# Optimization experiments

Hardware: AMD Instinct MI355X
Metric: run time of the kernel (lower is better)

## Reference

```python
import jax, jax.numpy as jnp
import numpy as np

IN_F = 4096
OUT_F = 11008

def setup_inputs() -> dict:
    key = jax.random.key(0)
    k1, k2, k3, k4 = jax.random.split(key, 4)
    x = jax.random.normal(k1, (4, 128, IN_F), dtype=jnp.float32)
    # int8-style quantized weights stored as int32 in [-127, 127]
    quantized_weight = jax.random.randint(k2, (OUT_F, IN_F), -127, 128, dtype=jnp.int32)
    # per-output-row scale, kept away from zero
    scale = jax.random.uniform(k3, (OUT_F, 1), dtype=jnp.float32, minval=0.5, maxval=1.5)
    bias = jax.random.normal(k4, (OUT_F,), dtype=jnp.float32)
    return {"x": x, "quantized_weight": quantized_weight, "scale": scale, "bias": bias}

def reference(x, quantized_weight, scale, bias):
    # int8 dequantization: weight = q.float() / scale  -> [OUT_F, IN_F] fp32
    weight = quantized_weight.astype(jnp.float32) / scale
    # F.linear(x, weight, bias) == x @ weight.T + bias
    out = jnp.einsum('bsi,oi->bso', x, weight) + bias
    return out
```

## Files before the change

### kernel.cpp

```cpp
#include <hip/hip_runtime.h>
#include <hip/hip_bf16.h>
#include <stdint.h>

#define IN_F  4096
#define OUT_F 11008
#define MTOT  512

#define BM 128
#define BN 64
#define BK 64
#define NKT (IN_F / BK)
#define A_TILE_B (BM * BK * 2)
#define B_TILE_B (BN * BK * 2)
#define X_WS_BYTES ((size_t)MTOT * IN_F * 2)

typedef __attribute__((ext_vector_type(4))) float  f32x4;
typedef __attribute__((ext_vector_type(4))) int    i32x4;
typedef __attribute__((ext_vector_type(2))) unsigned u32x2;
typedef __attribute__((ext_vector_type(4))) unsigned u32x4;
typedef __attribute__((ext_vector_type(8))) __bf16 bf16x8;

__device__ __forceinline__ unsigned pack2bf16_rnd(float lo, float hi) {
    unsigned ulo = __builtin_bit_cast(unsigned, lo) + 0x8000u;
    unsigned uhi = __builtin_bit_cast(unsigned, hi) + 0x8000u;
    return __builtin_amdgcn_perm(uhi, ulo, 0x07060302u);
}
__device__ __forceinline__ unsigned pack2bf16_exact(float lo, float hi) {
    return __builtin_amdgcn_perm(__builtin_bit_cast(unsigned, hi),
                                 __builtin_bit_cast(unsigned, lo), 0x07060302u);
}

__device__ __forceinline__ void gload_lds16(const void* g, void* l) {
    __builtin_amdgcn_global_load_lds(
        (const __attribute__((address_space(1))) unsigned*)g,
        (__attribute__((address_space(3))) unsigned*)l, 16, 0, 0);
}

#define BARRIER_VM(N) do {                                         \
    asm volatile("s_waitcnt vmcnt(" #N ") lgkmcnt(0)" ::: "memory"); \
    __builtin_amdgcn_s_barrier();                                  \
    __builtin_amdgcn_sched_barrier(0);                             \
} while (0)

__global__ __launch_bounds__(256)
void xconv_kernel(const float* __restrict__ X, char* __restrict__ xws) {
    const int gid  = blockIdx.x * 256 + threadIdx.x;
    const int row  = gid >> 9;
    const int col0 = (gid & 511) * 8;
    const float* src = X + (size_t)row * IN_F + col0;
    f32x4 v0 = *(const f32x4*)(src);
    f32x4 v1 = *(const f32x4*)(src + 4);
    u32x4 o;
    o.x = pack2bf16_rnd(v0.x, v0.y);
    o.y = pack2bf16_rnd(v0.z, v0.w);
    o.z = pack2bf16_rnd(v1.x, v1.y);
    o.w = pack2bf16_rnd(v1.z, v1.w);
    const int mtile = row >> 7, row_l = row & 127;
    const int kt = col0 >> 6,  k_l  = col0 & 63;
    const int a = row_l * 128 + k_l * 2;
    const int p = a ^ ((row_l & 7) << 4);
    *(u32x4*)(xws + (size_t)mtile * (NKT * A_TILE_B)
                  + (size_t)kt * A_TILE_B + p) = o;
}

__global__ __launch_bounds__(128, 2)
void qgemm_kernel(const char* __restrict__ xws,
                  const int*   __restrict__ W,
                  const float* __restrict__ scale,
                  const float* __restrict__ bias,
                  float* __restrict__ Out)
{
    __shared__ __align__(16) char smem[2 * (A_TILE_B + B_TILE_B)];
    char* bufA[2] = { smem,                smem + A_TILE_B };
    char* bufB[2] = { smem + 2 * A_TILE_B, smem + 2 * A_TILE_B + B_TILE_B };

    const int tid  = (int)threadIdx.x;
    const int lane = tid & 63;
    const int w    = tid >> 6;

    const int bid  = (int)blockIdx.x;
    const int lbid = (bid & 7) * 86 + (bid >> 3);
    const int mtile = lbid & 3;
    const int ntile = lbid >> 2;
    const int brow = mtile * BM;
    const int bcol = ntile * BN;

    const int srow  = tid >> 4;
    const int scol4 = tid & 15;
    const int* Wp = W + (size_t)(bcol + srow) * IN_F + scol4 * 4;

    const char* xsrc = xws + (size_t)mtile * (NKT * A_TILE_B)
                     + w * 8192 + lane * 16;

    i32x4 rbE[8], rbO[8];
    f32x4 acc[4][4];
    #pragma unroll
    for (int i = 0; i < 4; ++i)
        #pragma unroll
        for (int j = 0; j < 4; ++j)
            acc[i][j] = (f32x4){0.f, 0.f, 0.f, 0.f};

    #pragma unroll
    for (int k = 0; k < 8; ++k)
        rbE[k] = *(const i32x4*)(Wp + (size_t)(k * 8) * IN_F);
    #pragma unroll
    for (int k = 0; k < 8; ++k) {
        const int row = srow + k * 8;
        const int off = (row * 128 + scol4 * 8) ^ ((row & 7) << 4);
        u32x2 bv;
        bv.x = pack2bf16_exact((float)rbE[k].x, (float)rbE[k].y);
        bv.y = pack2bf16_exact((float)rbE[k].z, (float)rbE[k].w);
        *(u32x2*)(bufB[0] + off) = bv;
    }
    #pragma unroll
    for (int c = 0; c < 8; ++c)
        gload_lds16(xsrc + c * 1024, bufA[0] + w * 8192 + c * 1024);
    #pragma unroll
    for (int k = 0; k < 8; ++k)
        rbE[k] = *(const i32x4*)(Wp + BK + (size_t)(k * 8) * IN_F);
    BARRIER_VM(8);

    #define MFMA_PHASE(PB)                                                   \
        _Pragma("unroll")                                                    \
        for (int ks = 0; ks < 2; ++ks) {                                     \
            bf16x8 af[4], bfr[4];                                            \
            _Pragma("unroll")                                                \
            for (int mi = 0; mi < 4; ++mi) {                                 \
                const int row = w * 64 + mi * 16 + (lane & 15);              \
                const int off = (row * 128 + ks * 64 + (lane >> 4) * 16)     \
                                ^ ((row & 7) << 4);                          \
                af[mi] = *(const bf16x8*)(bufA[PB] + off);                   \
            }                                                                \
            _Pragma("unroll")                                                \
            for (int ni = 0; ni < 4; ++ni) {                                 \
                const int row = ni * 16 + (lane & 15);                       \
                const int off = (row * 128 + ks * 64 + (lane >> 4) * 16)     \
                                ^ ((row & 7) << 4);                          \
                bfr[ni] = *(const bf16x8*)(bufB[PB] + off);                  \
            }                                                                \
            _Pragma("unroll")                                                \
            for (int mi = 0; mi < 4; ++mi)                                   \
                _Pragma("unroll")                                            \
                for (int ni = 0; ni < 4; ++ni)                               \
                    acc[mi][ni] = __builtin_amdgcn_mfma_f32_16x16x32_bf16(   \
                        af[mi], bfr[ni], acc[mi][ni], 0, 0, 0);              \
        }

    #define CONVERT_B(RB, DSTB)                                              \
        _Pragma("unroll")                                                    \
        for (int k = 0; k < 8; ++k) {                                        \
            const int row = srow + k * 8;                                    \
            const int off = (row * 128 + scol4 * 8) ^ ((row & 7) << 4);      \
            u32x2 bv;                                                        \
            bv.x = pack2bf16_exact((float)RB[k].x, (float)RB[k].y);          \
            bv.y = pack2bf16_exact((float)RB[k].z, (float)RB[k].w);          \
            *(u32x2*)((DSTB) + off) = bv;                                    \
        }

    for (int kt2 = 0; kt2 < NKT; kt2 += 2) {
        const bool last_pair = (kt2 == NKT - 2);

        {
            const char* xs = xsrc + (size_t)(kt2 + 1) * A_TILE_B;
            #pragma unroll
            for (int c = 0; c < 8; ++c)
                gload_lds16(xs + c * 1024, bufA[1] + w * 8192 + c * 1024);
            if (!last_pair) {
                const int* Wk = Wp + (size_t)(kt2 + 2) * BK;
                #pragma unroll
                for (int k = 0; k < 8; ++k)
                    rbO[k] = *(const i32x4*)(Wk + (size_t)(k * 8) * IN_F);
            }
            CONVERT_B(rbE, bufB[1]);
            MFMA_PHASE(0);
            if (!last_pair) { BARRIER_VM(8); } else { BARRIER_VM(0); }
        }

        {
            if (!last_pair) {
                const char* xs = xsrc + (size_t)(kt2 + 2) * A_TILE_B;
                #pragma unroll
                for (int c = 0; c < 8; ++c)
                    gload_lds16(xs + c * 1024, bufA[0] + w * 8192 + c * 1024);
                const int* Wk = Wp + (size_t)(kt2 + 3) * BK;
                #pragma unroll
                for (int k = 0; k < 8; ++k)
                    rbE[k] = *(const i32x4*)(Wk + (size_t)(k * 8) * IN_F);
                CONVERT_B(rbO, bufB[0]);
            }
            MFMA_PHASE(1);
            if (!last_pair) { BARRIER_VM(8); }
        }
    }

    #pragma unroll
    for (int ni = 0; ni < 4; ++ni) {
        const int col = bcol + ni * 16 + (lane & 15);
        const float inv = 1.0f / scale[col];
        const float bs  = bias[col];
        #pragma unroll
        for (int mi = 0; mi < 4; ++mi) {
            const int row0 = brow + w * 64 + mi * 16 + ((lane >> 4) << 2);
            #pragma unroll
            for (int j = 0; j < 4; ++j)
                Out[(size_t)(row0 + j) * OUT_F + col] = acc[mi][ni][j] * inv + bs;
        }
    }
}

__global__ __launch_bounds__(128, 2)
void qgemm_fallback_kernel(const float* __restrict__ X,
                           const int*   __restrict__ W,
                           const float* __restrict__ scale,
                           const float* __restrict__ bias,
                           float* __restrict__ Out)
{
    __shared__ __align__(16) char smem[A_TILE_B + B_TILE_B];
    char* bufA = smem;
    char* bufB = smem + A_TILE_B;

    const int tid  = (int)threadIdx.x;
    const int lane = tid & 63;
    const int w    = tid >> 6;

    const int bid  = (int)blockIdx.x;
    const int lbid = (bid & 7) * 86 + (bid >> 3);
    const int mtile = lbid & 3;
    const int ntile = lbid >> 2;
    const int brow = mtile * BM;
    const int bcol = ntile * BN;

    const int srow  = tid >> 4;
    const int scol4 = tid & 15;
    const int* Wp = W + (size_t)(bcol + srow) * IN_F + scol4 * 4;
    const float* Xp = X + (size_t)(brow + srow) * IN_F + scol4 * 4;

    f32x4 acc[4][4];
    #pragma unroll
    for (int i = 0; i < 4; ++i)
        #pragma unroll
        for (int j = 0; j < 4; ++j)
            acc[i][j] = (f32x4){0.f, 0.f, 0.f, 0.f};

    for (int kt = 0; kt < NKT; ++kt) {
        #pragma unroll
        for (int k = 0; k < 8; ++k) {
            i32x4 rb = *(const i32x4*)(Wp + (size_t)kt * BK + (size_t)(k * 8) * IN_F);
            const int row = srow + k * 8;
            const int off = (row * 128 + scol4 * 8) ^ ((row & 7) << 4);
            u32x2 bv;
            bv.x = pack2bf16_exact((float)rb.x, (float)rb.y);
            bv.y = pack2bf16_exact((float)rb.z, (float)rb.w);
            *(u32x2*)(bufB + off) = bv;
        }
        #pragma unroll
        for (int k = 0; k < 16; ++k) {
            f32x4 ra = *(const f32x4*)(Xp + (size_t)kt * BK + (size_t)(k * 8) * IN_F);
            const int row = srow + k * 8;
            const int off = (row * 128 + scol4 * 8) ^ ((row & 7) << 4);
            u32x2 av;
            av.x = pack2bf16_rnd(ra.x, ra.y);
            av.y = pack2bf16_rnd(ra.z, ra.w);
            *(u32x2*)(bufA + off) = av;
        }
        __syncthreads();
        #pragma unroll
        for (int ks = 0; ks < 2; ++ks) {
            bf16x8 af[4], bfr[4];
            #pragma unroll
            for (int mi = 0; mi < 4; ++mi) {
                const int row = w * 64 + mi * 16 + (lane & 15);
                const int off = (row * 128 + ks * 64 + (lane >> 4) * 16)
                                ^ ((row & 7) << 4);
                af[mi] = *(const bf16x8*)(bufA + off);
            }
            #pragma unroll
            for (int ni = 0; ni < 4; ++ni) {
                const int row = ni * 16 + (lane & 15);
                const int off = (row * 128 + ks * 64 + (lane >> 4) * 16)
                                ^ ((row & 7) << 4);
                bfr[ni] = *(const bf16x8*)(bufB + off);
            }
            #pragma unroll
            for (int mi = 0; mi < 4; ++mi)
                #pragma unroll
                for (int ni = 0; ni < 4; ++ni)
                    acc[mi][ni] = __builtin_amdgcn_mfma_f32_16x16x32_bf16(
                        af[mi], bfr[ni], acc[mi][ni], 0, 0, 0);
        }
        __syncthreads();
    }

    #pragma unroll
    for (int ni = 0; ni < 4; ++ni) {
        const int col = bcol + ni * 16 + (lane & 15);
        const float inv = 1.0f / scale[col];
        const float bs  = bias[col];
        #pragma unroll
        for (int mi = 0; mi < 4; ++mi) {
            const int row0 = brow + w * 64 + mi * 16 + ((lane >> 4) << 2);
            #pragma unroll
            for (int j = 0; j < 4; ++j)
                Out[(size_t)(row0 + j) * OUT_F + col] = acc[mi][ni][j] * inv + bs;
        }
    }
}

extern "C" void kernel_launch(void* const* d_in, const int* in_sizes, int n_in,
                              void* d_out, int out_size, void* d_ws, size_t ws_size,
                              hipStream_t stream) {
    const float* X     = (const float*)d_in[0];
    const int*   W     = (const int*)d_in[1];
    const float* scale = (const float*)d_in[2];
    const float* bias  = (const float*)d_in[3];
    float* Out = (float*)d_out;

    const int grid = (MTOT / BM) * (OUT_F / BN);

    if (ws_size >= X_WS_BYTES) {
        char* xws = (char*)d_ws;
        xconv_kernel<<<(MTOT * IN_F / 8) / 256, 256, 0, stream>>>(X, xws);
        qgemm_kernel<<<grid, 128, 0, stream>>>(xws, W, scale, bias, Out);
    } else {
        qgemm_fallback_kernel<<<grid, 128, 0, stream>>>(X, W, scale, bias, Out);
    }
}
```

Baseline: 85.71 us.

## Store X in MFMA-fragment order and load A directly to registers, bypassing LDS

The X conversion kernel now writes bf16 activations in per-lane MFMA fragment order, so each wave can load its A fragments straight from global memory into registers with coalesced 16-byte loads. The A tiles and their async global-to-LDS copies are removed from the GEMM, leaving LDS only for the double-buffered B (int32 weights converted to bf16). This cuts LDS traffic and shared memory per block and drops the vmcnt-based waits. In exchange it needs 16 more VGPRs of A fragments per buffer, and the A global loads now sit directly on the MFMA critical path with no LDS staging.

```diff
diff --git a/kernel.cpp b/kernel.cpp
--- a/kernel.cpp
+++ b/kernel.cpp
@@ -10,8 +10,8 @@
 #define BN 64
 #define BK 64
 #define NKT (IN_F / BK)
-#define A_TILE_B (BM * BK * 2)
 #define B_TILE_B (BN * BK * 2)
+#define XT_B 16384
 #define X_WS_BYTES ((size_t)MTOT * IN_F * 2)
 
 typedef __attribute__((ext_vector_type(4))) float  f32x4;
@@ -30,14 +30,8 @@
                                  __builtin_bit_cast(unsigned, lo), 0x07060302u);
 }
 
-__device__ __forceinline__ void gload_lds16(const void* g, void* l) {
-    __builtin_amdgcn_global_load_lds(
-        (const __attribute__((address_space(1))) unsigned*)g,
-        (__attribute__((address_space(3))) unsigned*)l, 16, 0, 0);
-}
-
-#define BARRIER_VM(N) do {                                         \
-    asm volatile("s_waitcnt vmcnt(" #N ") lgkmcnt(0)" ::: "memory"); \
+#define BAR() do {                                                 \
+    asm volatile("s_waitcnt lgkmcnt(0)" ::: "memory");             \
     __builtin_amdgcn_s_barrier();                                  \
     __builtin_amdgcn_sched_barrier(0);                             \
 } while (0)
@@ -55,12 +49,15 @@
     o.y = pack2bf16_rnd(v0.z, v0.w);
     o.z = pack2bf16_rnd(v1.x, v1.y);
     o.w = pack2bf16_rnd(v1.z, v1.w);
-    const int mtile = row >> 7, row_l = row & 127;
-    const int kt = col0 >> 6,  k_l  = col0 & 63;
-    const int a = row_l * 128 + k_l * 2;
-    const int p = a ^ ((row_l & 7) << 4);
-    *(u32x4*)(xws + (size_t)mtile * (NKT * A_TILE_B)
-                  + (size_t)kt * A_TILE_B + p) = o;
+    const int mtile = row >> 7, mrow = row & 127;
+    const int mi = mrow >> 4,  l15 = mrow & 15;
+    const int kt  = col0 >> 6;
+    const int ks  = (col0 >> 5) & 1;
+    const int lhi = (col0 >> 3) & 3;
+    const int lane = lhi * 16 + l15;
+    const int f = mi * 2 + ks;
+    *(u32x4*)(xws + ((size_t)(mtile * NKT + kt) * 16 + f) * 1024
+                  + lane * 16) = o;
 }
 
 __global__ __launch_bounds__(128, 2)
@@ -70,9 +67,9 @@
                   const float* __restrict__ bias,
                   float* __restrict__ Out)
 {
-    __shared__ __align__(16) char smem[2 * (A_TILE_B + B_TILE_B)];
-    char* bufA[2] = { smem,                smem + A_TILE_B };
-    char* bufB[2] = { smem + 2 * A_TILE_B, smem + 2 * A_TILE_B + B_TILE_B };
+    __shared__ __align__(16) char smem[2 * B_TILE_B];
+    char* bufB0 = smem;
+    char* bufB1 = smem + B_TILE_B;
 
     const int tid  = (int)threadIdx.x;
     const int lane = tid & 63;
@@ -89,10 +86,10 @@
     const int scol4 = tid & 15;
     const int* Wp = W + (size_t)(bcol + srow) * IN_F + scol4 * 4;
 
-    const char* xsrc = xws + (size_t)mtile * (NKT * A_TILE_B)
-                     + w * 8192 + lane * 16;
-
-    i32x4 rbE[8], rbO[8];
+    const char* xAw = xws + (size_t)mtile * (NKT * XT_B) + w * 8192 + lane * 16;
+
+    i32x4 rb[8];
+    bf16x8 afE[8], afO[8];
     f32x4 acc[4][4];
     #pragma unroll
     for (int i = 0; i < 4; ++i)
@@ -100,97 +97,69 @@
         for (int j = 0; j < 4; ++j)
             acc[i][j] = (f32x4){0.f, 0.f, 0.f, 0.f};
 
-    #pragma unroll
-    for (int k = 0; k < 8; ++k)
-        rbE[k] = *(const i32x4*)(Wp + (size_t)(k * 8) * IN_F);
-    #pragma unroll
-    for (int k = 0; k < 8; ++k) {
-        const int row = srow + k * 8;
-        const int off = (row * 128 + scol4 * 8) ^ ((row & 7) << 4);
-        u32x2 bv;
-        bv.x = pack2bf16_exact((float)rbE[k].x, (float)rbE[k].y);
-        bv.y = pack2bf16_exact((float)rbE[k].z, (float)rbE[k].w);
-        *(u32x2*)(bufB[0] + off) = bv;
-    }
-    #pragma unroll
-    for (int c = 0; c < 8; ++c)
-        gload_lds16(xsrc + c * 1024, bufA[0] + w * 8192 + c * 1024);
-    #pragma unroll
-    for (int k = 0; k < 8; ++k)
-        rbE[k] = *(const i32x4*)(Wp + BK + (size_t)(k * 8) * IN_F);
-    BARRIER_VM(8);
-
-    #define MFMA_PHASE(PB)                                                   \
+    #define LOAD_A(AF, KT)                                                   \
+        _Pragma("unroll")                                                    \
+        for (int q = 0; q < 8; ++q)                                          \
+            AF[q] = *(const bf16x8*)(xAw + (size_t)(KT) * XT_B + q * 1024);
+
+    #define LOAD_B(KT)                                                       \
+        _Pragma("unroll")                                                    \
+        for (int k = 0; k < 8; ++k)                                          \
+            rb[k] = *(const i32x4*)(Wp + (size_t)(KT) * BK                   \
+                                       + (size_t)(k * 8) * IN_F);
+
+    #define CONVERT_B(DSTB)                                                  \
+        _Pragma("unroll")                                                    \
+        for (int k = 0; k < 8; ++k) {                                        \
+            const int row = srow + k * 8;                                    \
+            const int off = (row * 128 + scol4 * 8) ^ ((row & 7) << 4);      \
+            u32x2 bv;                                                        \
+            bv.x = pack2bf16_exact((float)rb[k].x, (float)rb[k].y);          \
+            bv.y = pack2bf16_exact((float)rb[k].z, (float)rb[k].w);          \
+            *(u32x2*)((DSTB) + off) = bv;                                    \
+        }
+
+    #define MFMA_PHASE(AF, BUFB)                                             \
         _Pragma("unroll")                                                    \
         for (int ks = 0; ks < 2; ++ks) {                                     \
-            bf16x8 af[4], bfr[4];                                            \
-            _Pragma("unroll")                                                \
-            for (int mi = 0; mi < 4; ++mi) {                                 \
-                const int row = w * 64 + mi * 16 + (lane & 15);              \
-                const int off = (row * 128 + ks * 64 + (lane >> 4) * 16)     \
-                                ^ ((row & 7) << 4);                          \
-                af[mi] = *(const bf16x8*)(bufA[PB] + off);                   \
-            }                                                                \
+            bf16x8 bfr[4];                                                   \
             _Pragma("unroll")                                                \
             for (int ni = 0; ni < 4; ++ni) {                                 \
                 const int row = ni * 16 + (lane & 15);                       \
                 const int off = (row * 128 + ks * 64 + (lane >> 4) * 16)     \
                                 ^ ((row & 7) << 4);                          \
-                bfr[ni] = *(const bf16x8*)(bufB[PB] + off);                  \
+                bfr[ni] = *(const bf16x8*)((BUFB) + off);                    \
             }                                                                \
             _Pragma("unroll")                                                \
             for (int mi = 0; mi < 4; ++mi)                                   \
                 _Pragma("unroll")                                            \
                 for (int ni = 0; ni < 4; ++ni)                               \
                     acc[mi][ni] = __builtin_amdgcn_mfma_f32_16x16x32_bf16(   \
-                        af[mi], bfr[ni], acc[mi][ni], 0, 0, 0);              \
-        }
-
-    #define CONVERT_B(RB, DSTB)                                              \
-        _Pragma("unroll")                                                    \
-        for (int k = 0; k < 8; ++k) {                                        \
-            const int row = srow + k * 8;                                    \
-            const int off = (row * 128 + scol4 * 8) ^ ((row & 7) << 4);      \
-            u32x2 bv;                                                        \
-            bv.x = pack2bf16_exact((float)RB[k].x, (float)RB[k].y);          \
-            bv.y = pack2bf16_exact((float)RB[k].z, (float)RB[k].w);          \
-            *(u32x2*)((DSTB) + off) = bv;                                    \
-        }
+                        AF[mi * 2 + ks], bfr[ni], acc[mi][ni], 0, 0, 0);     \
+        }
+
+    LOAD_B(0);
+    CONVERT_B(bufB0);
+    LOAD_A(afE, 0);
+    LOAD_B(1);
+    BAR();
 
     for (int kt2 = 0; kt2 < NKT; kt2 += 2) {
-        const bool last_pair = (kt2 == NKT - 2);
-
-        {
-            const char* xs = xsrc + (size_t)(kt2 + 1) * A_TILE_B;
-            #pragma unroll
-            for (int c = 0; c < 8; ++c)
-                gload_lds16(xs + c * 1024, bufA[1] + w * 8192 + c * 1024);
-            if (!last_pair) {
-                const int* Wk = Wp + (size_t)(kt2 + 2) * BK;
-                #pragma unroll
-                for (int k = 0; k < 8; ++k)
-                    rbO[k] = *(const i32x4*)(Wk + (size_t)(k * 8) * IN_F);
-            }
-            CONVERT_B(rbE, bufB[1]);
-            MFMA_PHASE(0);
-            if (!last_pair) { BARRIER_VM(8); } else { BARRIER_VM(0); }
-        }
-
-        {
-            if (!last_pair) {
-                const char* xs = xsrc + (size_t)(kt2 + 2) * A_TILE_B;
-                #pragma unroll
-                for (int c = 0; c < 8; ++c)
-                    gload_lds16(xs + c * 1024, bufA[0] + w * 8192 + c * 1024);
-                const int* Wk = Wp + (size_t)(kt2 + 3) * BK;
-                #pragma unroll
-                for (int k = 0; k < 8; ++k)
-                    rbE[k] = *(const i32x4*)(Wk + (size_t)(k * 8) * IN_F);
-                CONVERT_B(rbO, bufB[0]);
-            }
-            MFMA_PHASE(1);
-            if (!last_pair) { BARRIER_VM(8); }
-        }
+        const bool last = (kt2 == NKT - 2);
+
+        LOAD_A(afO, kt2 + 1);
+        CONVERT_B(bufB1);
+        if (!last) LOAD_B(kt2 + 2);
+        MFMA_PHASE(afE, bufB0);
+        BAR();
+
+        if (!last) {
+            LOAD_A(afE, kt2 + 2);
+            CONVERT_B(bufB0);
+            LOAD_B(kt2 + 3);
+        }
+        MFMA_PHASE(afO, bufB1);
+        if (!last) BAR();
     }
 
     #pragma unroll
@@ -206,6 +175,11 @@
                 Out[(size_t)(row0 + j) * OUT_F + col] = acc[mi][ni][j] * inv + bs;
         }
     }
+
+    #undef LOAD_A
+    #undef LOAD_B
+    #undef CONVERT_B
+    #undef MFMA_PHASE
 }
 
 __global__ __launch_bounds__(128, 2)
@@ -215,9 +189,9 @@
                            const float* __restrict__ bias,
                            float* __restrict__ Out)
 {
-    __shared__ __align__(16) char smem[A_TILE_B + B_TILE_B];
+    __shared__ __align__(16) char smem[BM * BK * 2 + B_TILE_B];
     char* bufA = smem;
-    char* bufB = smem + A_TILE_B;
+    char* bufB = smem + BM * BK * 2;
 
     const int tid  = (int)threadIdx.x;
     const int lane = tid & 63;
```

Result: faster. 76.41 us (-10.9%).
